# Kernel tuning notes

Hardware: AMD Instinct MI355X
Metric: run time of the kernel (lower is better)

## Reference

```python
import jax, jax.numpy as jnp
import numpy as np

B, T, C = 4, 2048, 1024
HEADS = 16
HEAD_DIM = C // HEADS
WINDOW = 256


def setup_inputs() -> dict:
    key = jax.random.key(0)
    k1, k2, k3 = jax.random.split(key, 3)
    x = jax.random.normal(k1, (B, T, C), dtype=jnp.float32)
    # torch nn.Linear weights: [out_features, in_features]; scale like kaiming-uniform-ish
    W_qkv = jax.random.normal(k2, (3 * C, C), dtype=jnp.float32) * (1.0 / np.sqrt(C))
    W_proj = jax.random.normal(k3, (C, C), dtype=jnp.float32) * (1.0 / np.sqrt(C))
    return {"x": x, "W_qkv": W_qkv, "W_proj": W_proj}


def reference(x, W_qkv, W_proj):
    b, t, c = x.shape
    h, d = HEADS, HEAD_DIM
    qkv = x @ W_qkv.T  # [b,t,3c]
    q, k, v = jnp.split(qkv, 3, axis=-1)
    q = q.reshape(b, t, h, d).transpose(0, 2, 1, 3)  # [b,h,t,d]
    k = k.reshape(b, t, h, d).transpose(0, 2, 1, 3)
    v = v.reshape(b, t, h, d).transpose(0, 2, 1, 3)
    scale = 1.0 / jnp.sqrt(jnp.asarray(d, dtype=q.dtype))
    scores = jnp.einsum('bhqd,bhkd->bhqk', q, k) * scale  # [b,h,t,t]
    i = jnp.arange(t)[:, None]
    j = jnp.arange(t)[None, :]
    mask = (j <= i) & (j > i - WINDOW)  # sliding-window causal band
    scores = jnp.where(mask, scores, -jnp.inf)
    attn = jax.nn.softmax(scores, axis=-1)
    y = jnp.einsum('bhqk,bhkd->bhqd', attn, v)  # [b,h,t,d]
    y = y.transpose(0, 2, 1, 3).reshape(b, t, c)
    return y @ W_proj.T
```

## Files before the change

### kernel.cpp

```cpp
#include <hip/hip_runtime.h>
#include <hip/hip_bf16.h>
#include <math.h>

#define BB 4
#define TT 2048
#define CC 1024
#define HH 16
#define DD 64
#define WW 256
#define MM (BB*TT)
#define NX (MM*CC)
#define NQ (3*CC*CC)
#define NP (CC*CC)

typedef __bf16 bf16x8 __attribute__((ext_vector_type(8)));
typedef __bf16 bf16x4 __attribute__((ext_vector_type(4)));
typedef float  f32x4  __attribute__((ext_vector_type(4)));

__device__ __forceinline__ void async_cp16(const void* g, void* l) {
  __builtin_amdgcn_global_load_lds(
      (const __attribute__((address_space(1))) void*)g,
      (__attribute__((address_space(3))) void*)l, 16, 0, 0);
}

__device__ __forceinline__ unsigned short f2bf(float v) {
  __hip_bfloat16 h = __float2bfloat16(v);
  return *(unsigned short*)&h;
}

__global__ __launch_bounds__(256)
void prep(const float* __restrict__ x,
          const float* __restrict__ wq,
          const float* __restrict__ wp,
          __hip_bfloat16* __restrict__ wdst,
          unsigned short* __restrict__ Apk) {
  const int p = blockIdx.x;
  const int tid = threadIdx.x;
  if (p < 4096) {
    int i = (p * 256 + tid) * 4;
    const float* src; int off;
    if (i < NQ) { src = wq; off = i; }
    else        { src = wp; off = i - NQ; }
    float4 v = *(const float4*)(src + off);
    wdst[i + 0] = __float2bfloat16(v.x);
    wdst[i + 1] = __float2bfloat16(v.y);
    wdst[i + 2] = __float2bfloat16(v.z);
    wdst[i + 3] = __float2bfloat16(v.w);
    return;
  }
  __shared__ __align__(16) unsigned short tile[64 * 72];
  const int pid = p - 4096;
  const int bm = pid & 127;
  const int bk = pid >> 7;
  const int tr = tid >> 4;
  const int tc = (tid & 15) * 4;
#pragma unroll
  for (int i = 0; i < 4; i++) {
    int row = i * 16 + tr;
    float4 v = *(const float4*)&x[(size_t)(bm * 64 + row) * 1024 + bk * 64 + tc];
    tile[row * 72 + tc + 0] = f2bf(v.x);
    tile[row * 72 + tc + 1] = f2bf(v.y);
    tile[row * 72 + tc + 2] = f2bf(v.z);
    tile[row * 72 + tc + 3] = f2bf(v.w);
  }
  __syncthreads();
  const int w = tid >> 6, lane = tid & 63;
  const int quad = lane >> 4, l15 = lane & 15;
#pragma unroll
  for (int f = 0; f < 2; f++) {
    bf16x8 fr = *(const bf16x8*)&tile[(w * 16 + l15) * 72 + f * 32 + quad * 8];
    *(bf16x8*)&Apk[(((size_t)(bm * 4 + w) * 32) + bk * 2 + f) * 512 + lane * 8] = fr;
  }
}

__global__ __launch_bounds__(512, 2)
void gemm_qkv(const unsigned short* __restrict__ Apk,
              const unsigned short* __restrict__ Bw,
              unsigned short* __restrict__ Qh,
              unsigned short* __restrict__ Kh,
              unsigned short* __restrict__ Vh) {
  __shared__ __align__(16) unsigned short Bs0[16 * 1024];
  __shared__ __align__(16) unsigned short Bs1[16 * 1024];

  const int id   = blockIdx.x;
  const int xcd  = id & 7;
  const int slot = id >> 3;
  const int mblk = slot / 3;
  const int nloc = slot % 3;
  const int n0 = (xcd * 3 + nloc) * 128;
  const int m0 = mblk * 256;

  const int tid  = threadIdx.x;
  const int w    = tid >> 6;
  const int lane = tid & 63;
  const int quad = lane >> 4;
  const int l15  = lane & 15;
  const int wm = w & 3;
  const int wn = w >> 2;

  f32x4 acc[4][4];
#pragma unroll
  for (int i = 0; i < 4; i++)
#pragma unroll
    for (int j = 0; j < 4; j++) acc[i][j] = (f32x4)0.0f;

  const unsigned short* abase =
      Apk + ((size_t)((m0 >> 4) + wm * 4) * 32) * 512 + lane * 8;

  auto stageB = [&](int k0, unsigned short* bs) {
#pragma unroll
    for (int i = 0; i < 4; i++) {
      int idx  = w + 8 * i;
      int kc   = idx >> 1;
      int half = idx & 1;
      async_cp16(Bw + (size_t)(n0 + half * 64 + lane) * 1024 + k0 + kc * 8,
                 &bs[kc * 1024 + half * 512]);
    }
  };

  bf16x8 Af[3][4];
  auto loadA = [&](int g, bf16x8* fr) {
#pragma unroll
    for (int tm = 0; tm < 4; tm++)
      fr[tm] = *(const bf16x8*)(abase + ((size_t)(tm * 32 + g)) * 512);
  };

  loadA(0, Af[0]);
  loadA(1, Af[1]);
  stageB(0, Bs0);
  __syncthreads();

#pragma unroll
  for (int s = 0; s < 8; s++) {
    const unsigned short* bs = (s & 1) ? Bs1 : Bs0;
    if (s + 1 < 8) stageB((s + 1) * 128, (s & 1) ? Bs0 : Bs1);
#pragma unroll
    for (int sub = 0; sub < 4; sub++) {
      const int g = s * 4 + sub;
      if (g + 2 < 32) loadA(g + 2, Af[(g + 2) % 3]);
      const bf16x8* af = Af[g % 3];
      bf16x8 bfv[4];
#pragma unroll
      for (int tn = 0; tn < 4; tn++)
        bfv[tn] = *(const bf16x8*)
            &bs[(sub * 4 + quad) * 1024 + (wn * 64 + tn * 16 + l15) * 8];
#pragma unroll
      for (int tm = 0; tm < 4; tm++)
#pragma unroll
        for (int tn = 0; tn < 4; tn++)
          acc[tm][tn] = __builtin_amdgcn_mfma_f32_16x16x32_bf16(
              af[tm], bfv[tn], acc[tm][tn], 0, 0, 0);
    }
    __syncthreads();
  }

#pragma unroll
  for (int tm = 0; tm < 4; tm++)
#pragma unroll
    for (int tn = 0; tn < 4; tn++) {
      int colb = n0 + wn * 64 + tn * 16;
      int t3 = colb >> 10;
      int hh = (colb >> 6) & 15;
      int dd = (colb & 63) + l15;
      unsigned short* dst = (t3 == 0) ? Qh : ((t3 == 1) ? Kh : Vh);
      float sc = (t3 == 0) ? 0.125f : 1.0f;
#pragma unroll
      for (int r = 0; r < 4; r++) {
        int row = m0 + wm * 64 + tm * 16 + quad * 4 + r;
        int b = row >> 11, tt = row & 2047;
        dst[((size_t)((b * 16 + hh) * 2048 + tt)) * 64 + dd] =
            f2bf(acc[tm][tn][r] * sc);
      }
    }
}

__global__ __launch_bounds__(512, 2)
void gemm_proj(const unsigned short* __restrict__ Apk,
               const unsigned short* __restrict__ Bw,
               float* __restrict__ Co) {
  __shared__ __align__(16) unsigned short Bs0[16 * 1024];
  __shared__ __align__(16) unsigned short Bs1[16 * 1024];

  const int id = blockIdx.x;
  const int n0 = (id & 7) * 128;
  const int m0 = (id >> 3) * 256;

  const int tid  = threadIdx.x;
  const int w    = tid >> 6;
  const int lane = tid & 63;
  const int quad = lane >> 4;
  const int l15  = lane & 15;
  const int wm = w & 3;
  const int wn = w >> 2;

  f32x4 acc[4][4];
#pragma unroll
  for (int i = 0; i < 4; i++)
#pragma unroll
    for (int j = 0; j < 4; j++) acc[i][j] = (f32x4)0.0f;

  const unsigned short* abase =
      Apk + ((size_t)((m0 >> 4) + wm * 4) * 32) * 512 + lane * 8;

  auto stageB = [&](int k0, unsigned short* bs) {
#pragma unroll
    for (int i = 0; i < 4; i++) {
      int idx  = w + 8 * i;
      int kc   = idx >> 1;
      int half = idx & 1;
      async_cp16(Bw + (size_t)(n0 + half * 64 + lane) * 1024 + k0 + kc * 8,
                 &bs[kc * 1024 + half * 512]);
    }
  };

  bf16x8 Af[3][4];
  auto loadA = [&](int g, bf16x8* fr) {
#pragma unroll
    for (int tm = 0; tm < 4; tm++)
      fr[tm] = *(const bf16x8*)(abase + ((size_t)(tm * 32 + g)) * 512);
  };

  loadA(0, Af[0]);
  loadA(1, Af[1]);
  stageB(0, Bs0);
  __syncthreads();

#pragma unroll
  for (int s = 0; s < 8; s++) {
    const unsigned short* bs = (s & 1) ? Bs1 : Bs0;
    if (s + 1 < 8) stageB((s + 1) * 128, (s & 1) ? Bs0 : Bs1);
#pragma unroll
    for (int sub = 0; sub < 4; sub++) {
      const int g = s * 4 + sub;
      if (g + 2 < 32) loadA(g + 2, Af[(g + 2) % 3]);
      const bf16x8* af = Af[g % 3];
      bf16x8 bfv[4];
#pragma unroll
      for (int tn = 0; tn < 4; tn++)
        bfv[tn] = *(const bf16x8*)
            &bs[(sub * 4 + quad) * 1024 + (wn * 64 + tn * 16 + l15) * 8];
#pragma unroll
      for (int tm = 0; tm < 4; tm++)
#pragma unroll
        for (int tn = 0; tn < 4; tn++)
          acc[tm][tn] = __builtin_amdgcn_mfma_f32_16x16x32_bf16(
              af[tm], bfv[tn], acc[tm][tn], 0, 0, 0);
    }
    __syncthreads();
  }

#pragma unroll
  for (int tm = 0; tm < 4; tm++)
#pragma unroll
    for (int tn = 0; tn < 4; tn++)
#pragma unroll
      for (int r = 0; r < 4; r++) {
        int row = m0 + wm * 64 + tm * 16 + quad * 4 + r;
        int col = n0 + wn * 64 + tn * 16 + l15;
        Co[(size_t)row * 1024 + col] = acc[tm][tn][r];
      }
}

__global__ __launch_bounds__(256)
void transpose_v(const unsigned short* __restrict__ Vh,
                 unsigned short* __restrict__ Vt) {
  __shared__ __align__(16) unsigned short tile[64 * 72];
  const int tid = threadIdx.x;
  const int tc = blockIdx.x, bh = blockIdx.y;
  const unsigned short* src = Vh + ((size_t)bh * 2048 + (size_t)tc * 64) * 64;
  for (int i = tid; i < 512; i += 256) {
    int r = i >> 3, ds = (i & 7) * 8;
    *(uint4*)&tile[r * 72 + ds] = *(const uint4*)&src[(size_t)r * 64 + ds];
  }
  __syncthreads();
  unsigned short* dst = Vt + (size_t)(bh * 32 + tc) * 4096;
  for (int i = tid; i < 512; i += 256) {
    int d = i >> 3, ts = (i & 7) * 8;
    unsigned int w0 = tile[(ts + 0) * 72 + d] | ((unsigned int)tile[(ts + 1) * 72 + d] << 16);
    unsigned int w1 = tile[(ts + 2) * 72 + d] | ((unsigned int)tile[(ts + 3) * 72 + d] << 16);
    unsigned int w2 = tile[(ts + 4) * 72 + d] | ((unsigned int)tile[(ts + 5) * 72 + d] << 16);
    unsigned int w3 = tile[(ts + 6) * 72 + d] | ((unsigned int)tile[(ts + 7) * 72 + d] << 16);
    uint4 o; o.x = w0; o.y = w1; o.z = w2; o.w = w3;
    *(uint4*)&dst[(size_t)d * 64 + ts] = o;
  }
}

__global__ __launch_bounds__(256, 2)
void attn_mfma(const unsigned short* __restrict__ Qh,
               const unsigned short* __restrict__ Kh,
               const unsigned short* __restrict__ Vt,
               unsigned short* __restrict__ Ypk) {
  __shared__ __align__(16) unsigned short SH[40960];

  const int tid  = threadIdx.x;
  const int w    = tid >> 6;
  const int lane = tid & 63;
  const int quad = lane >> 4;
  const int l15  = lane & 15;
  const int q0 = blockIdx.x * 64;
  const int bh = blockIdx.y;

  const int c0 = (q0 >= 256) ? 0 : (4 - (q0 >> 6));

  const unsigned short* Qg = Qh + ((size_t)bh * 2048 + q0) * 64;
  bf16x8 Qf[2];
#pragma unroll
  for (int fs = 0; fs < 2; fs++)
    Qf[fs] = *(const bf16x8*)(Qg + (w * 16 + l15) * 64 + fs * 32 + quad * 8);

  const unsigned short* Kg = Kh + (size_t)bh * 2048 * 64;
  const unsigned short* Vg = Vt + (size_t)bh * 32 * 4096;
  for (int ch = c0; ch < 5; ch++) {
    int sc = q0 - 256 + ch * 64;
#pragma unroll
    for (int i = 0; i < 2; i++) {
      int kc = w * 2 + i;
      async_cp16(Kg + (size_t)(sc + lane) * 64 + kc * 8,
                 &SH[ch * 4096 + kc * 512]);
      async_cp16(Vg + (size_t)(sc >> 6) * 4096 + lane * 64 + kc * 8,
                 &SH[20480 + ch * 4096 + kc * 512]);
    }
  }
  __syncthreads();

  f32x4 S[5][4];
#pragma unroll
  for (int ch = 0; ch < 5; ch++)
#pragma unroll
    for (int tn = 0; tn < 4; tn++) S[ch][tn] = (f32x4)0.0f;

#pragma unroll
  for (int ch = 0; ch < 5; ch++) {
    if (ch < c0) continue;
#pragma unroll
    for (int ks = 0; ks < 2; ks++) {
      int kc = ks * 4 + quad;
#pragma unroll
      for (int tn = 0; tn < 4; tn++) {
        bf16x8 bk = *(const bf16x8*)
            &SH[ch * 4096 + kc * 512 + (tn * 16 + l15) * 8];
        S[ch][tn] = __builtin_amdgcn_mfma_f32_16x16x32_bf16(
            Qf[ks], bk, S[ch][tn], 0, 0, 0);
      }
    }
  }

  const int qb = q0 + w * 16 + quad * 4;
  if (c0 == 0) {
#pragma unroll
    for (int tn = 0; tn < 4; tn++) {
      int j = q0 - 256 + tn * 16 + l15;
#pragma unroll
      for (int r = 0; r < 4; r++)
        if (qb + r > j + (WW - 1)) S[0][tn][r] = -__builtin_inff();
    }
  }
#pragma unroll
  for (int tn = 0; tn < 4; tn++) {
    int j = q0 + tn * 16 + l15;
#pragma unroll
    for (int r = 0; r < 4; r++)
      if (j > qb + r) S[4][tn][r] = -__builtin_inff();
  }

  float mrow[4], lrow[4];
#pragma unroll
  for (int r = 0; r < 4; r++) mrow[r] = -__builtin_inff();
#pragma unroll
  for (int ch = 0; ch < 5; ch++) {
    if (ch < c0) continue;
#pragma unroll
    for (int tn = 0; tn < 4; tn++)
#pragma unroll
      for (int r = 0; r < 4; r++)
        mrow[r] = fmaxf(mrow[r], S[ch][tn][r]);
  }
#pragma unroll
  for (int off = 1; off < 16; off <<= 1)
#pragma unroll
    for (int r = 0; r < 4; r++)
      mrow[r] = fmaxf(mrow[r], __shfl_xor(mrow[r], off));

#pragma unroll
  for (int r = 0; r < 4; r++) lrow[r] = 0.0f;
#pragma unroll
  for (int ch = 0; ch < 5; ch++) {
    if (ch < c0) continue;
#pragma unroll
    for (int tn = 0; tn < 4; tn++)
#pragma unroll
      for (int r = 0; r < 4; r++) {
        float e = __expf(S[ch][tn][r] - mrow[r]);
        S[ch][tn][r] = e;
        lrow[r] += e;
      }
  }
#pragma unroll
  for (int off = 1; off < 16; off <<= 1)
#pragma unroll
    for (int r = 0; r < 4; r++) lrow[r] += __shfl_xor(lrow[r], off);

  __syncthreads();

  f32x4 Oacc[4];
#pragma unroll
  for (int td = 0; td < 4; td++) Oacc[td] = (f32x4)0.0f;

#pragma unroll
  for (int ch = 0; ch < 5; ch++) {
    if (ch < c0) continue;
    unsigned short* Ps = SH + (ch & 1) * 4608;
#pragma unroll
    for (int tn = 0; tn < 4; tn++)
#pragma unroll
      for (int r = 0; r < 4; r++)
        Ps[(w * 16 + quad * 4 + r) * 68 + tn * 16 + l15] = f2bf(S[ch][tn][r]);
    asm volatile("s_waitcnt lgkmcnt(0)" ::: "memory");
#pragma unroll
    for (int ks = 0; ks < 2; ks++) {
      int off = (w * 16 + l15) * 68 + ks * 32 + quad * 8;
      bf16x4 plo = *(const bf16x4*)&Ps[off];
      bf16x4 phi = *(const bf16x4*)&Ps[off + 4];
      bf16x8 ap = __builtin_shufflevector(plo, phi, 0, 1, 2, 3, 4, 5, 6, 7);
      int kc = ks * 4 + quad;
#pragma unroll
      for (int td = 0; td < 4; td++) {
        bf16x8 bv = *(const bf16x8*)
            &SH[20480 + ch * 4096 + kc * 512 + (td * 16 + l15) * 8];
        Oacc[td] = __builtin_amdgcn_mfma_f32_16x16x32_bf16(
            ap, bv, Oacc[td], 0, 0, 0);
      }
    }
  }

  const int b = bh >> 4, h = bh & 15;
  float inv[4];
#pragma unroll
  for (int r = 0; r < 4; r++) inv[r] = 1.0f / lrow[r];
  unsigned short* Ot = SH + 10240;
#pragma unroll
  for (int td = 0; td < 4; td++)
#pragma unroll
    for (int r = 0; r < 4; r++)
      Ot[(w * 16 + quad * 4 + r) * 72 + td * 16 + l15] =
          f2bf(Oacc[td][r] * inv[r]);
  asm volatile("s_waitcnt lgkmcnt(0)" ::: "memory");
  const size_t rt = (size_t)((b * 2048 + q0) >> 4) + w;
#pragma unroll
  for (int f = 0; f < 2; f++) {
    bf16x8 fr = *(const bf16x8*)&Ot[(w * 16 + l15) * 72 + f * 32 + quad * 8];
    *(bf16x8*)&Ypk[(rt * 32 + h * 2 + f) * 512 + lane * 8] = fr;
  }
}

extern "C" void kernel_launch(void* const* d_in, const int* in_sizes, int n_in,
                              void* d_out, int out_size, void* d_ws, size_t ws_size,
                              hipStream_t stream) {
  const float* x     = (const float*)d_in[0];
  const float* wqkv  = (const float*)d_in[1];
  const float* wproj = (const float*)d_in[2];
  float* out = (float*)d_out;

  char* ws = (char*)d_ws;
  unsigned short* apk    = (unsigned short*)(ws);
  unsigned short* vtb    = (unsigned short*)(ws);
  unsigned short* wqkvb  = (unsigned short*)(ws + (size_t)16 * 1024 * 1024);
  unsigned short* wprojb = (unsigned short*)(ws + (size_t)22 * 1024 * 1024);
  unsigned short* qh     = (unsigned short*)(ws + (size_t)24 * 1024 * 1024);
  unsigned short* kh     = (unsigned short*)(ws + (size_t)40 * 1024 * 1024);
  unsigned short* vh     = (unsigned short*)(ws + (size_t)56 * 1024 * 1024);
  unsigned short* ypk    = (unsigned short*)(ws + (size_t)72 * 1024 * 1024);

  prep<<<4096 + 2048, 256, 0, stream>>>(
      x, wqkv, wproj, (__hip_bfloat16*)wqkvb, apk);

  gemm_qkv<<<768, 512, 0, stream>>>(apk, wqkvb, qh, kh, vh);

  transpose_v<<<dim3(32, 64), 256, 0, stream>>>(vh, vtb);

  attn_mfma<<<dim3(TT / 64, BB * HH), 256, 0, stream>>>(
      qh, kh, vtb, ypk);

  gemm_proj<<<256, 512, 0, stream>>>(ypk, wprojb, out);
}
```

Measured before the change: 245.3 us.

## Use 4-wave blocks with wider per-wave N tiles in QKV and projection GEMMs

```diff
diff --git a/kernel.cpp b/kernel.cpp
--- a/kernel.cpp
+++ b/kernel.cpp
@@ -73,7 +73,7 @@
   }
 }
 
-__global__ __launch_bounds__(512, 2)
+__global__ __launch_bounds__(256, 2)
 void gemm_qkv(const unsigned short* __restrict__ Apk,
               const unsigned short* __restrict__ Bw,
               unsigned short* __restrict__ Qh,
@@ -95,22 +95,20 @@
   const int lane = tid & 63;
   const int quad = lane >> 4;
   const int l15  = lane & 15;
-  const int wm = w & 3;
-  const int wn = w >> 2;
-
-  f32x4 acc[4][4];
+
+  f32x4 acc[4][8];
 #pragma unroll
   for (int i = 0; i < 4; i++)
 #pragma unroll
-    for (int j = 0; j < 4; j++) acc[i][j] = (f32x4)0.0f;
+    for (int j = 0; j < 8; j++) acc[i][j] = (f32x4)0.0f;
 
   const unsigned short* abase =
-      Apk + ((size_t)((m0 >> 4) + wm * 4) * 32) * 512 + lane * 8;
+      Apk + ((size_t)((m0 >> 4) + w * 4) * 32) * 512 + lane * 8;
 
   auto stageB = [&](int k0, unsigned short* bs) {
 #pragma unroll
-    for (int i = 0; i < 4; i++) {
-      int idx  = w + 8 * i;
+    for (int i = 0; i < 8; i++) {
+      int idx  = w + 4 * i;
       int kc   = idx >> 1;
       int half = idx & 1;
       async_cp16(Bw + (size_t)(n0 + half * 64 + lane) * 1024 + k0 + kc * 8,
@@ -118,7 +116,7 @@
     }
   };
 
-  bf16x8 Af[3][4];
+  bf16x8 Af[2][4];
   auto loadA = [&](int g, bf16x8* fr) {
 #pragma unroll
     for (int tm = 0; tm < 4; tm++)
@@ -126,7 +124,6 @@
   };
 
   loadA(0, Af[0]);
-  loadA(1, Af[1]);
   stageB(0, Bs0);
   __syncthreads();
 
@@ -137,19 +134,17 @@
 #pragma unroll
     for (int sub = 0; sub < 4; sub++) {
       const int g = s * 4 + sub;
-      if (g + 2 < 32) loadA(g + 2, Af[(g + 2) % 3]);
-      const bf16x8* af = Af[g % 3];
-      bf16x8 bfv[4];
-#pragma unroll
-      for (int tn = 0; tn < 4; tn++)
-        bfv[tn] = *(const bf16x8*)
-            &bs[(sub * 4 + quad) * 1024 + (wn * 64 + tn * 16 + l15) * 8];
-#pragma unroll
-      for (int tm = 0; tm < 4; tm++)
-#pragma unroll
-        for (int tn = 0; tn < 4; tn++)
+      if (g + 1 < 32) loadA(g + 1, Af[(g + 1) & 1]);
+      const bf16x8* af = Af[g & 1];
+#pragma unroll
+      for (int tn = 0; tn < 8; tn++) {
+        bf16x8 bfv = *(const bf16x8*)
+            &bs[(sub * 4 + quad) * 1024 + (tn * 16 + l15) * 8];
+#pragma unroll
+        for (int tm = 0; tm < 4; tm++)
           acc[tm][tn] = __builtin_amdgcn_mfma_f32_16x16x32_bf16(
-              af[tm], bfv[tn], acc[tm][tn], 0, 0, 0);
+              af[tm], bfv, acc[tm][tn], 0, 0, 0);
+      }
     }
     __syncthreads();
   }
@@ -157,8 +152,8 @@
 #pragma unroll
   for (int tm = 0; tm < 4; tm++)
 #pragma unroll
-    for (int tn = 0; tn < 4; tn++) {
-      int colb = n0 + wn * 64 + tn * 16;
+    for (int tn = 0; tn < 8; tn++) {
+      int colb = n0 + tn * 16;
       int t3 = colb >> 10;
       int hh = (colb >> 6) & 15;
       int dd = (colb & 63) + l15;
@@ -166,7 +161,7 @@
       float sc = (t3 == 0) ? 0.125f : 1.0f;
 #pragma unroll
       for (int r = 0; r < 4; r++) {
-        int row = m0 + wm * 64 + tm * 16 + quad * 4 + r;
+        int row = m0 + w * 64 + tm * 16 + quad * 4 + r;
         int b = row >> 11, tt = row & 2047;
         dst[((size_t)((b * 16 + hh) * 2048 + tt)) * 64 + dd] =
             f2bf(acc[tm][tn][r] * sc);
@@ -174,7 +169,7 @@
     }
 }
 
-__global__ __launch_bounds__(512, 2)
+__global__ __launch_bounds__(256, 2)
 void gemm_proj(const unsigned short* __restrict__ Apk,
                const unsigned short* __restrict__ Bw,
                float* __restrict__ Co) {
@@ -183,29 +178,27 @@
 
   const int id = blockIdx.x;
   const int n0 = (id & 7) * 128;
-  const int m0 = (id >> 3) * 256;
+  const int m0 = (id >> 3) * 128;
 
   const int tid  = threadIdx.x;
   const int w    = tid >> 6;
   const int lane = tid & 63;
   const int quad = lane >> 4;
   const int l15  = lane & 15;
-  const int wm = w & 3;
-  const int wn = w >> 2;
-
-  f32x4 acc[4][4];
-#pragma unroll
-  for (int i = 0; i < 4; i++)
-#pragma unroll
-    for (int j = 0; j < 4; j++) acc[i][j] = (f32x4)0.0f;
+
+  f32x4 acc[2][8];
+#pragma unroll
+  for (int i = 0; i < 2; i++)
+#pragma unroll
+    for (int j = 0; j < 8; j++) acc[i][j] = (f32x4)0.0f;
 
   const unsigned short* abase =
-      Apk + ((size_t)((m0 >> 4) + wm * 4) * 32) * 512 + lane * 8;
+      Apk + ((size_t)((m0 >> 4) + w * 2) * 32) * 512 + lane * 8;
 
   auto stageB = [&](int k0, unsigned short* bs) {
 #pragma unroll
-    for (int i = 0; i < 4; i++) {
-      int idx  = w + 8 * i;
+    for (int i = 0; i < 8; i++) {
+      int idx  = w + 4 * i;
       int kc   = idx >> 1;
       int half = idx & 1;
       async_cp16(Bw + (size_t)(n0 + half * 64 + lane) * 1024 + k0 + kc * 8,
@@ -213,15 +206,14 @@
     }
   };
 
-  bf16x8 Af[3][4];
+  bf16x8 Af[2][2];
   auto loadA = [&](int g, bf16x8* fr) {
 #pragma unroll
-    for (int tm = 0; tm < 4; tm++)
+    for (int tm = 0; tm < 2; tm++)
       fr[tm] = *(const bf16x8*)(abase + ((size_t)(tm * 32 + g)) * 512);
   };
 
   loadA(0, Af[0]);
-  loadA(1, Af[1]);
   stageB(0, Bs0);
   __syncthreads();
 
@@ -232,31 +224,29 @@
 #pragma unroll
     for (int sub = 0; sub < 4; sub++) {
       const int g = s * 4 + sub;
-      if (g + 2 < 32) loadA(g + 2, Af[(g + 2) % 3]);
-      const bf16x8* af = Af[g % 3];
-      bf16x8 bfv[4];
-#pragma unroll
-      for (int tn = 0; tn < 4; tn++)
-        bfv[tn] = *(const bf16x8*)
-            &bs[(sub * 4 + quad) * 1024 + (wn * 64 + tn * 16 + l15) * 8];
-#pragma unroll
-      for (int tm = 0; tm < 4; tm++)
-#pragma unroll
-        for (int tn = 0; tn < 4; tn++)
+      if (g + 1 < 32) loadA(g + 1, Af[(g + 1) & 1]);
+      const bf16x8* af = Af[g & 1];
+#pragma unroll
+      for (int tn = 0; tn < 8; tn++) {
+        bf16x8 bfv = *(const bf16x8*)
+            &bs[(sub * 4 + quad) * 1024 + (tn * 16 + l15) * 8];
+#pragma unroll
+        for (int tm = 0; tm < 2; tm++)
           acc[tm][tn] = __builtin_amdgcn_mfma_f32_16x16x32_bf16(
-              af[tm], bfv[tn], acc[tm][tn], 0, 0, 0);
+              af[tm], bfv, acc[tm][tn], 0, 0, 0);
+      }
     }
     __syncthreads();
   }
 
 #pragma unroll
-  for (int tm = 0; tm < 4; tm++)
-#pragma unroll
-    for (int tn = 0; tn < 4; tn++)
+  for (int tm = 0; tm < 2; tm++)
+#pragma unroll
+    for (int tn = 0; tn < 8; tn++)
 #pragma unroll
       for (int r = 0; r < 4; r++) {
-        int row = m0 + wm * 64 + tm * 16 + quad * 4 + r;
-        int col = n0 + wn * 64 + tn * 16 + l15;
+        int row = m0 + w * 32 + tm * 16 + quad * 4 + r;
+        int col = n0 + tn * 16 + l15;
         Co[(size_t)row * 1024 + col] = acc[tm][tn][r];
       }
 }
@@ -474,12 +464,12 @@
   prep<<<4096 + 2048, 256, 0, stream>>>(
       x, wqkv, wproj, (__hip_bfloat16*)wqkvb, apk);
 
-  gemm_qkv<<<768, 512, 0, stream>>>(apk, wqkvb, qh, kh, vh);
+  gemm_qkv<<<768, 256, 0, stream>>>(apk, wqkvb, qh, kh, vh);
 
   transpose_v<<<dim3(32, 64), 256, 0, stream>>>(vh, vtb);
 
   attn_mfma<<<dim3(TT / 64, BB * HH), 256, 0, stream>>>(
       qh, kh, vtb, ypk);
 
-  gemm_proj<<<256, 512, 0, stream>>>(ypk, wprojb, out);
-}
+  gemm_proj<<<512, 256, 0, stream>>>(ypk, wprojb, out);
+}
```

Result: faster. 238.7 us (-2.7%).
